# Kernel optimization log

Measured on AMD Instinct MI355X. Metric: run time of the kernel, lower is better.

Reference implementation:

```python
import jax, jax.numpy as jnp
import numpy as np

N = 1048576
DIM = 2
HID = 64
E = 4


def setup_inputs() -> dict:
    key = jax.random.key(0)
    ks = jax.random.split(key, 10)
    s_in = 1.0 / np.sqrt(DIM)
    s_hid = 1.0 / np.sqrt(HID)
    return {
        "x": jax.random.normal(ks[0], (N, DIM), dtype=jnp.float32),
        # router: Linear(dim -> E)
        "rW": jax.random.uniform(ks[1], (DIM, E), minval=-s_in, maxval=s_in, dtype=jnp.float32),
        "rb": jax.random.uniform(ks[2], (E,), minval=-s_in, maxval=s_in, dtype=jnp.float32),
        # stacked expert weights: Linear(dim->hid), Linear(hid->hid), Linear(hid->dim)
        "w1": jax.random.uniform(ks[3], (E, DIM, HID), minval=-s_in, maxval=s_in, dtype=jnp.float32),
        "b1": jax.random.uniform(ks[4], (E, HID), minval=-s_in, maxval=s_in, dtype=jnp.float32),
        "w2": jax.random.uniform(ks[5], (E, HID, HID), minval=-s_hid, maxval=s_hid, dtype=jnp.float32),
        "b2": jax.random.uniform(ks[6], (E, HID), minval=-s_hid, maxval=s_hid, dtype=jnp.float32),
        "w3": jax.random.uniform(ks[7], (E, HID, DIM), minval=-s_hid, maxval=s_hid, dtype=jnp.float32),
        "b3": jax.random.uniform(ks[8], (E, DIM), minval=-s_hid, maxval=s_hid, dtype=jnp.float32),
    }


def reference(x, rW, rb, w1, b1, w2, b2, w3, b3):
    # Router: hard top-1 via argmax, exactly as torch.argmax(router_logits, -1)
    router_logits = x @ rW + rb                       # [N, E]
    best = jnp.argmax(router_logits, axis=-1)         # [N]

    # Compute all experts densely (vectorized replacement of the masked loop),
    # then select the winning expert's output per token via one-hot.
    h = jax.nn.relu(jnp.einsum('nd,edh->enh', x, w1) + b1[:, None, :])   # [E, N, HID]
    h = jax.nn.relu(jnp.einsum('enh,ehk->enk', h, w2) + b2[:, None, :])  # [E, N, HID]
    y = jnp.einsum('enh,ehd->end', h, w3) + b3[:, None, :]               # [E, N, DIM]

    onehot = jax.nn.one_hot(best, E, dtype=x.dtype)   # [N, E]
    out = jnp.einsum('end,ne->nd', y, onehot)         # [N, DIM]
    return out, router_logits
```

## Files before the change

### kernel.cpp

```cpp
#include <hip/hip_runtime.h>

#define NTOK 1048576
#define HID 64
#define TPB 256
#define TPB_TOK 1024
#define RPT (TPB_TOK / TPB)
#define NBLK (NTOK / TPB_TOK)
#define MAXSLOT (TPB_TOK + 64)
#define MAXTILE (TPB_TOK / 16 + 4)

typedef _Float16 half8 __attribute__((ext_vector_type(8)));
typedef _Float16 half2v __attribute__((ext_vector_type(2)));
typedef float f32x4 __attribute__((ext_vector_type(4)));

static __device__ __forceinline__ half2v pkh(float a, float b) {
    return __builtin_bit_cast(half2v, __builtin_amdgcn_cvt_pkrtz(a, b));
}

__global__ void prep_w2_frag(const float* __restrict__ w2, _Float16* __restrict__ wsf) {
    int idx  = blockIdx.x * 256 + threadIdx.x;
    int j    = idx & 7;
    int lane = (idx >> 3) & 63;
    int ks   = (idx >> 9) & 1;
    int mt   = (idx >> 10) & 3;
    int e    = idx >> 12;
    int kin  = ks * 32 + (lane >> 4) * 8 + j;
    int m    = mt * 16 + (lane & 15);
    wsf[idx] = (_Float16)w2[(e * HID + kin) * HID + m];
}

__global__ __launch_bounds__(TPB, 4) void moe_kernel(
    const float* __restrict__ x, const float* __restrict__ rW, const float* __restrict__ rb,
    const float* __restrict__ w1, const float* __restrict__ b1,
    const float* __restrict__ b2,
    const float* __restrict__ w3, const float* __restrict__ b3,
    const _Float16* __restrict__ wsf, float* __restrict__ out)
{
    __shared__ float2 xs[MAXSLOT];
    __shared__ float2 ysh[MAXSLOT];
    __shared__ int wcnt[4][4];
    __shared__ int seg_start[4], cumt[5];
    __shared__ unsigned tmap[MAXTILE];

    const int t = threadIdx.x, w = t >> 6, lane = t & 63;
    const int base = blockIdx.x * TPB_TOK;
    const unsigned long long lt = (1ull << lane) - 1ull;

    const float r00 = rW[0], r01 = rW[1], r02 = rW[2], r03 = rW[3];
    const float r10 = rW[4], r11 = rW[5], r12 = rW[6], r13 = rW[7];
    const float rb0 = rb[0], rb1 = rb[1], rb2 = rb[2], rb3 = rb[3];

    int c0 = 0, c1 = 0, c2 = 0, c3 = 0;
    int slotl[RPT]; int bestl[RPT]; float2 xv_[RPT]; int slotf[RPT];
    float* logits_out = out + 2 * NTOK;
    #pragma unroll
    for (int i = 0; i < RPT; i++) {
        int tok = base + i * TPB + t;
        float2 xv = ((const float2*)x)[tok];
        float l0 = xv.x * r00 + xv.y * r10 + rb0;
        float l1 = xv.x * r01 + xv.y * r11 + rb1;
        float l2 = xv.x * r02 + xv.y * r12 + rb2;
        float l3 = xv.x * r03 + xv.y * r13 + rb3;
        ((float4*)logits_out)[tok] = make_float4(l0, l1, l2, l3);
        int b = 0; float bv = l0;
        if (l1 > bv) { bv = l1; b = 1; }
        if (l2 > bv) { bv = l2; b = 2; }
        if (l3 > bv) { bv = l3; b = 3; }
        unsigned long long m0 = __ballot(b == 0), m1 = __ballot(b == 1),
                           m2 = __ballot(b == 2), m3 = __ballot(b == 3);
        unsigned long long mym = (b == 0) ? m0 : (b == 1) ? m1 : (b == 2) ? m2 : m3;
        int cb = (b == 0) ? c0 : (b == 1) ? c1 : (b == 2) ? c2 : c3;
        slotl[i] = cb + __popcll(mym & lt);
        bestl[i] = b; xv_[i] = xv;
        c0 += __popcll(m0); c1 += __popcll(m1); c2 += __popcll(m2); c3 += __popcll(m3);
    }
    if (lane < 4) wcnt[w][lane] = (lane == 0) ? c0 : (lane == 1) ? c1 : (lane == 2) ? c2 : c3;
    __syncthreads();
    if (t == 0) {
        int run = 0, ct = 0; cumt[0] = 0;
        for (int e = 0; e < 4; e++) {
            int c = wcnt[0][e] + wcnt[1][e] + wcnt[2][e] + wcnt[3][e];
            seg_start[e] = run;
            run += (c + 15) & ~15; ct += (c + 15) >> 4; cumt[e + 1] = ct;
        }
    }
    __syncthreads();
    int wo0 = 0, wo1 = 0, wo2 = 0, wo3 = 0;
    for (int ww = 0; ww < w; ww++) {
        wo0 += wcnt[ww][0]; wo1 += wcnt[ww][1]; wo2 += wcnt[ww][2]; wo3 += wcnt[ww][3];
    }
    #pragma unroll
    for (int i = 0; i < RPT; i++) {
        int b = bestl[i];
        int wo = (b == 0) ? wo0 : (b == 1) ? wo1 : (b == 2) ? wo2 : wo3;
        int slot = seg_start[b] + wo + slotl[i];
        xs[slot] = xv_[i];
        slotf[i] = slot;
    }
    int T = cumt[4];
    for (int g = t; g < T; g += TPB) {
        int e = (g >= cumt[1]) + (g >= cumt[2]) + (g >= cumt[3]);
        int i = g - cumt[e];
        int row = seg_start[e] + 16 * i;
        tmap[g] = (unsigned)e | ((unsigned)row << 2);
    }
    __syncthreads();

    const int q = lane >> 4, n16 = lane & 15;
    int chunk = (T + 3) >> 2;
    int g0 = w * chunk, g1 = g0 + chunk; if (g1 > T) g1 = T;

    half2v w1h0[8], w1h1[8], b1h[8];
    half8 w2A[4][2];
    half2v b2h[4][2];
    half2v w3h[4][4];
    float2 b3r = make_float2(0.f, 0.f);
    int cur_e = -1;
    const half2v hz = { (_Float16)0, (_Float16)0 };

    unsigned tm_n = 0; float2 xv_n = make_float2(0.f, 0.f);
    if (g0 < g1) {
        tm_n = tmap[g0];
        xv_n = xs[((tm_n >> 2) & 0xFFF) + n16];
    }

    for (int g = g0; g < g1; g++) {
        unsigned tm = tm_n; float2 xv = xv_n;
        if (g + 1 < g1) {
            tm_n = tmap[g + 1];
            xv_n = xs[((tm_n >> 2) & 0xFFF) + n16];
        }
        int e   = tm & 3;
        int row = (tm >> 2) & 0xFFF;
        if (e != cur_e) {
            cur_e = e;
            const float* base0 = w1 + e * 128;
            const float* base1 = w1 + e * 128 + 64;
            const float* baseb = b1 + e * 64;
            #pragma unroll
            for (int p = 0; p < 4; p++) {
                float2 a0 = *(const float2*)(base0 + q * 8 + 2 * p);
                float2 a1 = *(const float2*)(base0 + 32 + q * 8 + 2 * p);
                w1h0[p]     = pkh(a0.x, a0.y);
                w1h0[4 + p] = pkh(a1.x, a1.y);
                float2 c0_ = *(const float2*)(base1 + q * 8 + 2 * p);
                float2 c1_ = *(const float2*)(base1 + 32 + q * 8 + 2 * p);
                w1h1[p]     = pkh(c0_.x, c0_.y);
                w1h1[4 + p] = pkh(c1_.x, c1_.y);
                float2 d0 = *(const float2*)(baseb + q * 8 + 2 * p);
                float2 d1 = *(const float2*)(baseb + 32 + q * 8 + 2 * p);
                b1h[p]     = pkh(d0.x, d0.y);
                b1h[4 + p] = pkh(d1.x, d1.y);
            }
            #pragma unroll
            for (int mt = 0; mt < 4; mt++) {
                w2A[mt][0] = ((const half8*)wsf)[((e * 4 + mt) * 2 + 0) * 64 + lane];
                w2A[mt][1] = ((const half8*)wsf)[((e * 4 + mt) * 2 + 1) * 64 + lane];
                float4 bb = ((const float4*)(b2 + e * 64))[mt * 4 + q];
                b2h[mt][0] = pkh(bb.x, bb.y);
                b2h[mt][1] = pkh(bb.z, bb.w);
                #pragma unroll
                for (int i = 0; i < 4; i++) {
                    int r = mt * 16 + q * 4 + i;
                    float2 wv = ((const float2*)(w3 + e * 128))[r];
                    w3h[mt][i] = pkh(wv.x, wv.y);
                }
            }
            b3r = ((const float2*)b3)[e];
        }
        half2v xh0 = pkh(xv.x, xv.x);
        half2v xh1 = pkh(xv.y, xv.y);
        half8 bf0, bf1;
        #pragma unroll
        for (int p = 0; p < 4; p++) {
            half2v ha = w1h0[p] * xh0 + w1h1[p] * xh1 + b1h[p];
            half2v hb = w1h0[4 + p] * xh0 + w1h1[4 + p] * xh1 + b1h[4 + p];
            ha = __builtin_elementwise_max(ha, hz);
            hb = __builtin_elementwise_max(hb, hz);
            bf0[2 * p] = ha.x; bf0[2 * p + 1] = ha.y;
            bf1[2 * p] = hb.x; bf1[2 * p + 1] = hb.y;
        }
        half2v ya = hz, yb = hz;
        #pragma unroll
        for (int mt = 0; mt < 4; mt++) {
            f32x4 acc = {0.f, 0.f, 0.f, 0.f};
            acc = __builtin_amdgcn_mfma_f32_16x16x32_f16(w2A[mt][0], bf0, acc, 0, 0, 0);
            acc = __builtin_amdgcn_mfma_f32_16x16x32_f16(w2A[mt][1], bf1, acc, 0, 0, 0);
            half2v h01 = __builtin_elementwise_max(pkh(acc[0], acc[1]) + b2h[mt][0], hz);
            half2v h23 = __builtin_elementwise_max(pkh(acc[2], acc[3]) + b2h[mt][1], hz);
            half2v h0s = { h01.x, h01.x }, h1s = { h01.y, h01.y };
            half2v h2s = { h23.x, h23.x }, h3s = { h23.y, h23.y };
            half2v* acc01 = (mt & 2) ? &yb : &ya;
            *acc01 = *acc01 + h0s * w3h[mt][0];
            *acc01 = *acc01 + h1s * w3h[mt][1];
            *acc01 = *acc01 + h2s * w3h[mt][2];
            *acc01 = *acc01 + h3s * w3h[mt][3];
        }
        half2v yp = ya + yb;
        float yr = __builtin_bit_cast(float, yp);
        yp = yp + __builtin_bit_cast(half2v, __shfl_xor(yr, 16));
        yr = __builtin_bit_cast(float, yp);
        yp = yp + __builtin_bit_cast(half2v, __shfl_xor(yr, 32));
        if (q == 0) {
            ysh[row + n16] = make_float2((float)yp.x + b3r.x, (float)yp.y + b3r.y);
        }
    }
    __syncthreads();

    #pragma unroll
    for (int i = 0; i < RPT; i++) {
        ((float2*)out)[base + i * TPB + t] = ysh[slotf[i]];
    }
}

extern "C" void kernel_launch(void* const* d_in, const int* in_sizes, int n_in,
                              void* d_out, int out_size, void* d_ws, size_t ws_size,
                              hipStream_t stream) {
    const float* x  = (const float*)d_in[0];
    const float* rW = (const float*)d_in[1];
    const float* rb = (const float*)d_in[2];
    const float* w1 = (const float*)d_in[3];
    const float* b1 = (const float*)d_in[4];
    const float* w2 = (const float*)d_in[5];
    const float* b2 = (const float*)d_in[6];
    const float* w3 = (const float*)d_in[7];
    const float* b3 = (const float*)d_in[8];
    float* out = (float*)d_out;
    _Float16* wsf = (_Float16*)d_ws;

    hipLaunchKernelGGL(prep_w2_frag, dim3(64), dim3(256), 0, stream, w2, wsf);
    hipLaunchKernelGGL(moe_kernel, dim3(NBLK), dim3(TPB), 0, stream,
                       x, rW, rb, w1, b1, b2, w3, b3, (const _Float16*)wsf, out);
}
```

Measured before the change: 103.3 us.

## Stage expert weights in LDS, use fdot2 for layer 3, reuse xs buffer

```diff
diff --git a/kernel.cpp b/kernel.cpp
--- a/kernel.cpp
+++ b/kernel.cpp
@@ -10,11 +10,20 @@
 #define MAXTILE (TPB_TOK / 16 + 4)
 
 typedef _Float16 half8 __attribute__((ext_vector_type(8)));
+typedef _Float16 half4 __attribute__((ext_vector_type(4)));
 typedef _Float16 half2v __attribute__((ext_vector_type(2)));
 typedef float f32x4 __attribute__((ext_vector_type(4)));
 
 static __device__ __forceinline__ half2v pkh(float a, float b) {
     return __builtin_bit_cast(half2v, __builtin_amdgcn_cvt_pkrtz(a, b));
+}
+
+static __device__ __forceinline__ float fdot2f(half2v a, half2v b, float c) {
+#if __has_builtin(__builtin_amdgcn_fdot2)
+    return __builtin_amdgcn_fdot2(a, b, c, false);
+#else
+    return c + (float)a.x * (float)b.x + (float)a.y * (float)b.y;
+#endif
 }
 
 __global__ void prep_w2_frag(const float* __restrict__ w2, _Float16* __restrict__ wsf) {
@@ -37,14 +46,36 @@
     const _Float16* __restrict__ wsf, float* __restrict__ out)
 {
     __shared__ float2 xs[MAXSLOT];
-    __shared__ float2 ysh[MAXSLOT];
     __shared__ int wcnt[4][4];
     __shared__ int seg_start[4], cumt[5];
     __shared__ unsigned tmap[MAXTILE];
+    __shared__ __align__(16) half2v l_w1[4][2][32];
+    __shared__ __align__(16) half2v l_b1[4][32];
+    __shared__ __align__(16) half2v l_b2[4][32];
+    __shared__ __align__(16) half2v l_w3c[4][2][32];
+    __shared__ float2 l_b3[4];
 
     const int t = threadIdx.x, w = t >> 6, lane = t & 63;
     const int base = blockIdx.x * TPB_TOK;
     const unsigned long long lt = (1ull << lane) - 1ull;
+
+    {
+        int e = t >> 6, i = t & 63;
+        float2 v1 = ((const float2*)(w1 + e * 128))[i];
+        l_w1[e][i >> 5][i & 31] = pkh(v1.x, v1.y);
+        if (i < 32) {
+            float2 vb = ((const float2*)(b1 + e * 64))[i];
+            l_b1[e][i] = pkh(vb.x, vb.y);
+            float2 v2 = ((const float2*)(b2 + e * 64))[i];
+            l_b2[e][i] = pkh(v2.x, v2.y);
+        } else {
+            int ii = i - 32;
+            float4 wv = ((const float4*)(w3 + e * 128))[ii];
+            l_w3c[e][0][ii] = pkh(wv.x, wv.z);
+            l_w3c[e][1][ii] = pkh(wv.y, wv.w);
+        }
+        if (t < 4) l_b3[t] = ((const float2*)b3)[t];
+    }
 
     const float r00 = rW[0], r01 = rW[1], r02 = rW[2], r03 = rW[3];
     const float r10 = rW[4], r11 = rW[5], r12 = rW[6], r13 = rW[7];
@@ -110,13 +141,12 @@
     int chunk = (T + 3) >> 2;
     int g0 = w * chunk, g1 = g0 + chunk; if (g1 > T) g1 = T;
 
-    half2v w1h0[8], w1h1[8], b1h[8];
     half8 w2A[4][2];
-    half2v b2h[4][2];
-    half2v w3h[4][4];
     float2 b3r = make_float2(0.f, 0.f);
     int cur_e = -1;
     const half2v hz = { (_Float16)0, (_Float16)0 };
+    const half8 hz8 = { (_Float16)0, (_Float16)0, (_Float16)0, (_Float16)0,
+                        (_Float16)0, (_Float16)0, (_Float16)0, (_Float16)0 };
 
     unsigned tm_n = 0; float2 xv_n = make_float2(0.f, 0.f);
     if (g0 < g1) {
@@ -134,82 +164,59 @@
         int row = (tm >> 2) & 0xFFF;
         if (e != cur_e) {
             cur_e = e;
-            const float* base0 = w1 + e * 128;
-            const float* base1 = w1 + e * 128 + 64;
-            const float* baseb = b1 + e * 64;
-            #pragma unroll
-            for (int p = 0; p < 4; p++) {
-                float2 a0 = *(const float2*)(base0 + q * 8 + 2 * p);
-                float2 a1 = *(const float2*)(base0 + 32 + q * 8 + 2 * p);
-                w1h0[p]     = pkh(a0.x, a0.y);
-                w1h0[4 + p] = pkh(a1.x, a1.y);
-                float2 c0_ = *(const float2*)(base1 + q * 8 + 2 * p);
-                float2 c1_ = *(const float2*)(base1 + 32 + q * 8 + 2 * p);
-                w1h1[p]     = pkh(c0_.x, c0_.y);
-                w1h1[4 + p] = pkh(c1_.x, c1_.y);
-                float2 d0 = *(const float2*)(baseb + q * 8 + 2 * p);
-                float2 d1 = *(const float2*)(baseb + 32 + q * 8 + 2 * p);
-                b1h[p]     = pkh(d0.x, d0.y);
-                b1h[4 + p] = pkh(d1.x, d1.y);
-            }
             #pragma unroll
             for (int mt = 0; mt < 4; mt++) {
                 w2A[mt][0] = ((const half8*)wsf)[((e * 4 + mt) * 2 + 0) * 64 + lane];
                 w2A[mt][1] = ((const half8*)wsf)[((e * 4 + mt) * 2 + 1) * 64 + lane];
-                float4 bb = ((const float4*)(b2 + e * 64))[mt * 4 + q];
-                b2h[mt][0] = pkh(bb.x, bb.y);
-                b2h[mt][1] = pkh(bb.z, bb.w);
-                #pragma unroll
-                for (int i = 0; i < 4; i++) {
-                    int r = mt * 16 + q * 4 + i;
-                    float2 wv = ((const float2*)(w3 + e * 128))[r];
-                    w3h[mt][i] = pkh(wv.x, wv.y);
-                }
             }
-            b3r = ((const float2*)b3)[e];
-        }
-        half2v xh0 = pkh(xv.x, xv.x);
-        half2v xh1 = pkh(xv.y, xv.y);
-        half8 bf0, bf1;
-        #pragma unroll
-        for (int p = 0; p < 4; p++) {
-            half2v ha = w1h0[p] * xh0 + w1h1[p] * xh1 + b1h[p];
-            half2v hb = w1h0[4 + p] * xh0 + w1h1[4 + p] * xh1 + b1h[4 + p];
-            ha = __builtin_elementwise_max(ha, hz);
-            hb = __builtin_elementwise_max(hb, hz);
-            bf0[2 * p] = ha.x; bf0[2 * p + 1] = ha.y;
-            bf1[2 * p] = hb.x; bf1[2 * p + 1] = hb.y;
-        }
-        half2v ya = hz, yb = hz;
+            b3r = l_b3[e];
+        }
+        const int q4 = q * 4;
+        half8 wa_lo = *(const half8*)&l_w1[e][0][q4];
+        half8 wa_hi = *(const half8*)&l_w1[e][0][16 + q4];
+        half8 wb_lo = *(const half8*)&l_w1[e][1][q4];
+        half8 wb_hi = *(const half8*)&l_w1[e][1][16 + q4];
+        half8 b1lo  = *(const half8*)&l_b1[e][q4];
+        half8 b1hi  = *(const half8*)&l_b1[e][16 + q4];
+        _Float16 xa = (_Float16)xv.x, xb = (_Float16)xv.y;
+        half8 bf0 = wa_lo * xa + wb_lo * xb + b1lo;
+        half8 bf1 = wa_hi * xa + wb_hi * xb + b1hi;
+        bf0 = __builtin_elementwise_max(bf0, hz8);
+        bf1 = __builtin_elementwise_max(bf1, hz8);
+
+        float y0 = 0.f, y1 = 0.f;
         #pragma unroll
         for (int mt = 0; mt < 4; mt++) {
+            half4 b2v  = *(const half4*)&l_b2[e][mt * 8 + q * 2];
+            half4 w3c0 = *(const half4*)&l_w3c[e][0][mt * 8 + q * 2];
+            half4 w3c1 = *(const half4*)&l_w3c[e][1][mt * 8 + q * 2];
             f32x4 acc = {0.f, 0.f, 0.f, 0.f};
             acc = __builtin_amdgcn_mfma_f32_16x16x32_f16(w2A[mt][0], bf0, acc, 0, 0, 0);
             acc = __builtin_amdgcn_mfma_f32_16x16x32_f16(w2A[mt][1], bf1, acc, 0, 0, 0);
-            half2v h01 = __builtin_elementwise_max(pkh(acc[0], acc[1]) + b2h[mt][0], hz);
-            half2v h23 = __builtin_elementwise_max(pkh(acc[2], acc[3]) + b2h[mt][1], hz);
-            half2v h0s = { h01.x, h01.x }, h1s = { h01.y, h01.y };
-            half2v h2s = { h23.x, h23.x }, h3s = { h23.y, h23.y };
-            half2v* acc01 = (mt & 2) ? &yb : &ya;
-            *acc01 = *acc01 + h0s * w3h[mt][0];
-            *acc01 = *acc01 + h1s * w3h[mt][1];
-            *acc01 = *acc01 + h2s * w3h[mt][2];
-            *acc01 = *acc01 + h3s * w3h[mt][3];
-        }
-        half2v yp = ya + yb;
-        float yr = __builtin_bit_cast(float, yp);
-        yp = yp + __builtin_bit_cast(half2v, __shfl_xor(yr, 16));
-        yr = __builtin_bit_cast(float, yp);
-        yp = yp + __builtin_bit_cast(half2v, __shfl_xor(yr, 32));
+            half2v b2a = __builtin_shufflevector(b2v, b2v, 0, 1);
+            half2v b2b = __builtin_shufflevector(b2v, b2v, 2, 3);
+            half2v h01 = __builtin_elementwise_max(pkh(acc[0], acc[1]) + b2a, hz);
+            half2v h23 = __builtin_elementwise_max(pkh(acc[2], acc[3]) + b2b, hz);
+            half2v w30a = __builtin_shufflevector(w3c0, w3c0, 0, 1);
+            half2v w30b = __builtin_shufflevector(w3c0, w3c0, 2, 3);
+            half2v w31a = __builtin_shufflevector(w3c1, w3c1, 0, 1);
+            half2v w31b = __builtin_shufflevector(w3c1, w3c1, 2, 3);
+            y0 = fdot2f(h01, w30a, y0);
+            y0 = fdot2f(h23, w30b, y0);
+            y1 = fdot2f(h01, w31a, y1);
+            y1 = fdot2f(h23, w31b, y1);
+        }
+        y0 += __shfl_xor(y0, 16); y0 += __shfl_xor(y0, 32);
+        y1 += __shfl_xor(y1, 16); y1 += __shfl_xor(y1, 32);
         if (q == 0) {
-            ysh[row + n16] = make_float2((float)yp.x + b3r.x, (float)yp.y + b3r.y);
+            xs[row + n16] = make_float2(y0 + b3r.x, y1 + b3r.y);
         }
     }
     __syncthreads();
 
     #pragma unroll
     for (int i = 0; i < RPT; i++) {
-        ((float2*)out)[base + i * TPB + t] = ysh[slotf[i]];
+        ((float2*)out)[base + i * TPB + t] = xs[slotf[i]];
     }
 }
 
```

Result: no change. 103.1 us (-0.2%).
